# Optimization experiments

Hardware: AMD Instinct MI355X
Metric: run time of the kernel (lower is better)

## Reference

```python
import jax, jax.numpy as jnp
import numpy as np

N, D = 8192, 128

def setup_inputs() -> dict:
    key = jax.random.key(0)
    kq, kk, kv = jax.random.split(key, 3)
    return {
        "query": jax.random.normal(kq, (N, D), dtype=jnp.float32),
        "key": jax.random.normal(kk, (N, D), dtype=jnp.float32),
        "value": jax.random.normal(kv, (N, D), dtype=jnp.float32),
    }

def reference(query, key, value):
    # FlashAttentionV1 computes exact (non-causal, unmasked) softmax attention:
    # softmax(Q K^T / sqrt(d)) V, via tiled online softmax. The math is
    # identical to the dense formulation below.
    d = query.shape[-1]
    scores = jnp.einsum('qd,kd->qk', query, key) / jnp.sqrt(jnp.asarray(d, query.dtype))
    probs = jax.nn.softmax(scores, axis=-1)
    return jnp.einsum('qk,kd->qd', probs, value)
```

## Files before the change

### kernel.cpp

```cpp
#include <hip/hip_runtime.h>

#define NTOK 8192
#define DH   128
#define QBLK 128
#define KVB  64

typedef __attribute__((ext_vector_type(8)))  short bf16x8;
typedef __attribute__((ext_vector_type(16))) float f32x16;
typedef __attribute__((ext_vector_type(4)))  unsigned short u16x4;

typedef __attribute__((address_space(1))) const void gv_t;
typedef __attribute__((address_space(3))) void sv_t;

static __device__ __forceinline__ unsigned short f2bf(float x) {
  union { float f; unsigned int u; } a; a.f = x;
  unsigned int r = a.u + 0x7FFFu + ((a.u >> 16) & 1u);
  return (unsigned short)(r >> 16);
}

static __device__ __forceinline__ unsigned pk2(float lo, float hi) {
  unsigned r;
  asm("v_cvt_pk_bf16_f32 %0, %1, %2" : "=v"(r) : "v"(lo), "v"(hi));
  return r;
}

static __device__ __forceinline__ f32x16 zero16() {
  f32x16 v;
  #pragma unroll
  for (int i = 0; i < 16; ++i) v[i] = 0.f;
  return v;
}

__global__ __launch_bounds__(256)
void fa_prep(const float* __restrict__ Kg, const float* __restrict__ Vg,
             char* __restrict__ Kimg, char* __restrict__ Vimg)
{
  const int t = blockIdx.x;
  const int tid = threadIdx.x;

  {
    const int krow = tid >> 2;
    const int kcg  = (tid & 3) * 32;
    const float* src = Kg + ((size_t)t * KVB + krow) * DH + kcg;
    char* drow = Kimg + (size_t)t * 16384 + krow * 256;
    const int sw = (krow & 15) << 4;
    #pragma unroll
    for (int w = 0; w < 4; ++w) {
      float4 a = *reinterpret_cast<const float4*>(src + w * 8);
      float4 b = *reinterpret_cast<const float4*>(src + w * 8 + 4);
      union { bf16x8 v; unsigned short u[8]; } f;
      f.u[0] = f2bf(a.x); f.u[1] = f2bf(a.y); f.u[2] = f2bf(a.z); f.u[3] = f2bf(a.w);
      f.u[4] = f2bf(b.x); f.u[5] = f2bf(b.y); f.u[6] = f2bf(b.z); f.u[7] = f2bf(b.w);
      *reinterpret_cast<bf16x8*>(drow + ((kcg * 2 + w * 16) ^ sw)) = f.v;
    }
  }

  {
    #pragma unroll
    for (int it = 0; it < 2; ++it) {
      int task = tid + it * 256;
      int kvl  = (task & 15) * 4;
      int d0   = (task >> 4) * 4;
      const float* src = Vg + ((size_t)t * KVB + kvl) * DH + d0;
      float4 r0 = *reinterpret_cast<const float4*>(src);
      float4 r1 = *reinterpret_cast<const float4*>(src + DH);
      float4 r2 = *reinterpret_cast<const float4*>(src + 2 * DH);
      float4 r3 = *reinterpret_cast<const float4*>(src + 3 * DH);
      char* base = Vimg + (size_t)t * 16384;
      const int bb = kvl * 2;
      { int d = d0 + 0;
        u16x4 w4 = (u16x4){f2bf(r0.x), f2bf(r1.x), f2bf(r2.x), f2bf(r3.x)};
        *reinterpret_cast<u16x4*>(base + d * 128 + (bb ^ ((d & 15) << 3))) = w4; }
      { int d = d0 + 1;
        u16x4 w4 = (u16x4){f2bf(r0.y), f2bf(r1.y), f2bf(r2.y), f2bf(r3.y)};
        *reinterpret_cast<u16x4*>(base + d * 128 + (bb ^ ((d & 15) << 3))) = w4; }
      { int d = d0 + 2;
        u16x4 w4 = (u16x4){f2bf(r0.z), f2bf(r1.z), f2bf(r2.z), f2bf(r3.z)};
        *reinterpret_cast<u16x4*>(base + d * 128 + (bb ^ ((d & 15) << 3))) = w4; }
      { int d = d0 + 3;
        u16x4 w4 = (u16x4){f2bf(r0.w), f2bf(r1.w), f2bf(r2.w), f2bf(r3.w)};
        *reinterpret_cast<u16x4*>(base + d * 128 + (bb ^ ((d & 15) << 3))) = w4; }
    }
  }
}

static __device__ __forceinline__ void softmax_half(
    const f32x16& st, float& m_run, float& l_run, f32x16* oacc,
    bf16x8& pfa, bf16x8& pfb)
{
  float a0 = fmaxf(st[0],  st[1]),  a1 = fmaxf(st[2],  st[3]);
  float a2 = fmaxf(st[4],  st[5]),  a3 = fmaxf(st[6],  st[7]);
  float a4 = fmaxf(st[8],  st[9]),  a5 = fmaxf(st[10], st[11]);
  float a6 = fmaxf(st[12], st[13]), a7 = fmaxf(st[14], st[15]);
  float b0 = fmaxf(a0, a1), b1 = fmaxf(a2, a3);
  float b2 = fmaxf(a4, a5), b3 = fmaxf(a6, a7);
  float pmax = fmaxf(fmaxf(b0, b1), fmaxf(b2, b3));
  if (!__all(pmax <= m_run + 8.f)) {
    pmax = fmaxf(pmax, __shfl_xor(pmax, 32));
    const float m_new = fmaxf(m_run, pmax);
    const float corr  = (m_run > -1e30f) ? exp2f(m_run - m_new) : 0.f;
    l_run *= corr;
    #pragma unroll
    for (int i = 0; i < 4; ++i) oacc[i] = oacc[i] * corr;
    m_run = m_new;
  }
  float e[16];
  #pragma unroll
  for (int r = 0; r < 16; ++r) e[r] = exp2f(st[r] - m_run);
  float s0 = (e[0] + e[1])   + (e[2] + e[3]);
  float s1 = (e[4] + e[5])   + (e[6] + e[7]);
  float s2 = (e[8] + e[9])   + (e[10] + e[11]);
  float s3 = (e[12] + e[13]) + (e[14] + e[15]);
  l_run += (s0 + s1) + (s2 + s3);
  union { bf16x8 v; unsigned u[4]; } fa, fb;
  fa.u[0] = pk2(e[0],  e[1]);  fa.u[1] = pk2(e[2],  e[3]);
  fa.u[2] = pk2(e[4],  e[5]);  fa.u[3] = pk2(e[6],  e[7]);
  fb.u[0] = pk2(e[8],  e[9]);  fb.u[1] = pk2(e[10], e[11]);
  fb.u[2] = pk2(e[12], e[13]); fb.u[3] = pk2(e[14], e[15]);
  pfa = fa.v; pfb = fb.v;
}

__global__ __launch_bounds__(256, 2)
void fa_fwd(const float* __restrict__ Qg, const char* __restrict__ Kimg,
            const char* __restrict__ Vimg, float* __restrict__ Od,
            float* __restrict__ Mp, float* __restrict__ Lp,
            int ksplit, int chunk_len)
{
  __shared__ __align__(16) char smem[2][32768];
  const int tid  = threadIdx.x;
  const int lane = tid & 63;
  const int wv   = tid >> 6;
  const int l31  = lane & 31;
  const int hi   = lane >> 5;

  const int q0blk = blockIdx.x * QBLK;
  const int q     = q0blk + wv * 32 + l31;
  const int chunk = blockIdx.y;
  const float QSCALE = 0.1275313310087464f;

  const int tile0 = (chunk * chunk_len) >> 6;
  const int nst   = chunk_len >> 6;

  bf16x8 qf[8];
  {
    const float* qs = Qg + (size_t)q * DH + hi * 8;
    #pragma unroll
    for (int kc = 0; kc < 8; ++kc) {
      float4 a = *reinterpret_cast<const float4*>(qs + kc * 16);
      float4 b = *reinterpret_cast<const float4*>(qs + kc * 16 + 4);
      union { bf16x8 v; unsigned u[4]; } f;
      f.u[0] = pk2(a.x * QSCALE, a.y * QSCALE);
      f.u[1] = pk2(a.z * QSCALE, a.w * QSCALE);
      f.u[2] = pk2(b.x * QSCALE, b.y * QSCALE);
      f.u[3] = pk2(b.z * QSCALE, b.w * QSCALE);
      qf[kc] = f.v;
    }
  }

  const char* gbase = (wv < 2 ? Kimg : Vimg);
  const size_t goff = (size_t)(wv & 1) * 8192 + (size_t)lane * 16;
  const int    loff = (wv < 2 ? 0 : 16384) + (wv & 1) * 8192;

#define STAGE(B, T) do {                                                      \
    const char* _s = gbase + (size_t)(T) * 16384 + goff;                      \
    char* _d = &smem[B][loff];                                                \
    _Pragma("unroll")                                                         \
    for (int _i = 0; _i < 8; ++_i)                                            \
      __builtin_amdgcn_global_load_lds((gv_t*)(_s + _i * 1024),               \
                                       (sv_t*)(_d + _i * 1024), 16, 0, 0);    \
  } while (0)

  STAGE(0, tile0);
  if (nst > 1) STAGE(1, tile0 + 1);

  f32x16 oacc[4];
  #pragma unroll
  for (int i = 0; i < 4; ++i) oacc[i] = zero16();
  float m_run = -INFINITY, l_run = 0.f;

  int cur = 0;
  for (int t = 0; t < nst; ++t) {
    if (t + 1 < nst) asm volatile("s_waitcnt vmcnt(8)" ::: "memory");
    else             asm volatile("s_waitcnt vmcnt(0)" ::: "memory");
    __builtin_amdgcn_sched_barrier(0);
    __builtin_amdgcn_s_barrier();

    const char* smK = smem[cur];
    const char* smV = smem[cur] + 16384;
    const int swk = (l31 & 15) << 4;
    const int swv = (l31 & 15) << 3;

    f32x16 st0 = zero16(), st1 = zero16();
    __builtin_amdgcn_s_setprio(1);
    #pragma unroll
    for (int kc = 0; kc < 8; ++kc) {
      const int cb = (kc * 32 + hi * 16) ^ swk;
      bf16x8 a0 = *reinterpret_cast<const bf16x8*>(smK + l31 * 256 + cb);
      st0 = __builtin_amdgcn_mfma_f32_32x32x16_bf16(a0, qf[kc], st0, 0, 0, 0);
      bf16x8 a1 = *reinterpret_cast<const bf16x8*>(smK + (l31 + 32) * 256 + cb);
      st1 = __builtin_amdgcn_mfma_f32_32x32x16_bf16(a1, qf[kc], st1, 0, 0, 0);
    }
    __builtin_amdgcn_s_setprio(0);

    bf16x8 pf0a, pf0b;
    softmax_half(st0, m_run, l_run, oacc, pf0a, pf0b);
    __builtin_amdgcn_s_setprio(1);
    #pragma unroll
    for (int c = 0; c < 2; ++c) {
      const bf16x8 pb = c ? pf0b : pf0a;
      #pragma unroll
      for (int dt = 0; dt < 4; ++dt) {
        const char* vb = smV + (dt * 32 + l31) * 128;
        union { bf16x8 v; u16x4 h[2]; } a;
        a.h[0] = *reinterpret_cast<const u16x4*>(vb + ((c * 32 + 8 * hi) ^ swv));
        a.h[1] = *reinterpret_cast<const u16x4*>(vb + ((c * 32 + 16 + 8 * hi) ^ swv));
        oacc[dt] = __builtin_amdgcn_mfma_f32_32x32x16_bf16(a.v, pb, oacc[dt], 0, 0, 0);
      }
    }
    __builtin_amdgcn_s_setprio(0);

    bf16x8 pf1a, pf1b;
    softmax_half(st1, m_run, l_run, oacc, pf1a, pf1b);
    __builtin_amdgcn_s_setprio(1);
    #pragma unroll
    for (int c = 2; c < 4; ++c) {
      const bf16x8 pb = (c & 1) ? pf1b : pf1a;
      #pragma unroll
      for (int dt = 0; dt < 4; ++dt) {
        const char* vb = smV + (dt * 32 + l31) * 128;
        union { bf16x8 v; u16x4 h[2]; } a;
        a.h[0] = *reinterpret_cast<const u16x4*>(vb + ((c * 32 + 8 * hi) ^ swv));
        a.h[1] = *reinterpret_cast<const u16x4*>(vb + ((c * 32 + 16 + 8 * hi) ^ swv));
        oacc[dt] = __builtin_amdgcn_mfma_f32_32x32x16_bf16(a.v, pb, oacc[dt], 0, 0, 0);
      }
    }
    __builtin_amdgcn_s_setprio(0);

    __builtin_amdgcn_s_barrier();
    if (t + 2 < nst) STAGE(cur, tile0 + t + 2);
    cur ^= 1;
  }
#undef STAGE

  const float l_tot = l_run + __shfl_xor(l_run, 32);
  const float scale = (ksplit == 1) ? (1.f / l_tot) : 1.f;
  float* dstB = (ksplit == 1) ? Od : Od + (size_t)chunk * NTOK * DH;

  char* base = &smem[0][0] + wv * 16384;
  #pragma unroll
  for (int dt = 0; dt < 4; ++dt)
    #pragma unroll
    for (int rg = 0; rg < 4; ++rg)
      #pragma unroll
      for (int j = 0; j < 4; ++j) {
        const int d = dt * 32 + rg * 8 + hi * 4 + j;
        *reinterpret_cast<float*>(base + d * 128 + l31 * 4) =
            oacc[dt][rg * 4 + j] * scale;
      }
  asm volatile("s_waitcnt lgkmcnt(0)" ::: "memory");
  __builtin_amdgcn_sched_barrier(0);
  const int qloc4 = lane >> 2;
  const int s4    = lane & 3;
  #pragma unroll
  for (int qh = 0; qh < 2; ++qh) {
    const int qloc = qh * 16 + qloc4;
    float* dst = dstB + (size_t)(q0blk + wv * 32 + qloc) * DH;
    #pragma unroll
    for (int i = 0; i < 8; ++i) {
      const int dd = s4 * 4 + i * 16;
      float4 v;
      v.x = *reinterpret_cast<float*>(base + (dd + 0) * 128 + qloc * 4);
      v.y = *reinterpret_cast<float*>(base + (dd + 1) * 128 + qloc * 4);
      v.z = *reinterpret_cast<float*>(base + (dd + 2) * 128 + qloc * 4);
      v.w = *reinterpret_cast<float*>(base + (dd + 3) * 128 + qloc * 4);
      *reinterpret_cast<float4*>(dst + dd) = v;
    }
  }

  if (ksplit > 1 && lane < 32) {
    const int qg = q0blk + wv * 32 + lane;
    Mp[chunk * NTOK + qg] = m_run;
    Lp[chunk * NTOK + qg] = l_tot;
  }
}

__global__ __launch_bounds__(256)
void fa_combine(const float* __restrict__ Op, const float* __restrict__ Mp,
                const float* __restrict__ Lp, float* __restrict__ out, int ksplit)
{
  const int gid = blockIdx.x * 256 + threadIdx.x;
  const int q   = gid >> 5;
  const int dv  = (gid & 31) * 4;
  float mx = -INFINITY;
  for (int c = 0; c < ksplit; ++c) mx = fmaxf(mx, Mp[c * NTOK + q]);
  float den = 0.f;
  float ax = 0.f, ay = 0.f, az = 0.f, aw = 0.f;
  for (int c = 0; c < ksplit; ++c) {
    const float w = exp2f(Mp[c * NTOK + q] - mx);
    den += w * Lp[c * NTOK + q];
    float4 o = *reinterpret_cast<const float4*>(Op + (size_t)c * NTOK * DH + (size_t)q * DH + dv);
    ax += w * o.x; ay += w * o.y; az += w * o.z; aw += w * o.w;
  }
  const float r = 1.f / den;
  float4 res; res.x = ax * r; res.y = ay * r; res.z = az * r; res.w = aw * r;
  *reinterpret_cast<float4*>(out + (size_t)q * DH + dv) = res;
}

extern "C" void kernel_launch(void* const* d_in, const int* in_sizes, int n_in,
                              void* d_out, int out_size, void* d_ws, size_t ws_size,
                              hipStream_t stream)
{
  const float* Q = (const float*)d_in[0];
  const float* K = (const float*)d_in[1];
  const float* V = (const float*)d_in[2];
  float* out = (float*)d_out;

  auto need = [](size_t ks) {
    return ks * (size_t)NTOK * DH * 4 + 2 * ks * (size_t)NTOK * 4;
  };
  int KS = (ws_size >= need(8)) ? 8 : (ws_size >= need(4)) ? 4 : 2;

  char* Kimg = (char*)d_out;
  char* Vimg = Kimg + (size_t)NTOK * 256;

  float* Op = (float*)d_ws;
  float* Mp = Op + (size_t)KS * NTOK * DH;
  float* Lp = Mp + (size_t)KS * NTOK;

  fa_prep<<<NTOK / KVB, 256, 0, stream>>>(K, V, Kimg, Vimg);
  fa_fwd<<<dim3(NTOK / QBLK, KS), 256, 0, stream>>>(Q, Kimg, Vimg, Op, Mp, Lp,
                                                    KS, NTOK / KS);
  fa_combine<<<NTOK * DH / 4 / 256, 256, 0, stream>>>(Op, Mp, Lp, out, KS);
}
```

Baseline: 68.66 us.

## Shrink LDS to single-buffered V for 3 blocks/CU and raise KV split to 12

LDS per block drops from 64KB to 48KB by keeping K double-buffered and V single-buffered, with V loads issued one tile ahead and awaited by a mid-iteration barrier. Launch bounds go to 3 blocks per CU, and the KV split rises to 12 with uneven chunk sizes handled by a remainder-aware tile partition. Both softmax halves now run before a single PV MFMA phase, and the epilogue staging is serialized across wave pairs to fit the smaller LDS. The aim is more resident blocks and more grid parallelism. The cost is an extra barrier per tile, exposed V load latency, and more register pressure from the 3-block bound.

```diff
diff --git a/kernel.cpp b/kernel.cpp
--- a/kernel.cpp
+++ b/kernel.cpp
@@ -4,6 +4,7 @@
 #define DH   128
 #define QBLK 128
 #define KVB  64
+#define TILES (NTOK / KVB)
 
 typedef __attribute__((ext_vector_type(8)))  short bf16x8;
 typedef __attribute__((ext_vector_type(16))) float f32x16;
@@ -120,13 +121,12 @@
   pfa = fa.v; pfb = fb.v;
 }
 
-__global__ __launch_bounds__(256, 2)
+__global__ __launch_bounds__(256, 3)
 void fa_fwd(const float* __restrict__ Qg, const char* __restrict__ Kimg,
             const char* __restrict__ Vimg, float* __restrict__ Od,
-            float* __restrict__ Mp, float* __restrict__ Lp,
-            int ksplit, int chunk_len)
-{
-  __shared__ __align__(16) char smem[2][32768];
+            float* __restrict__ Mp, float* __restrict__ Lp, int ksplit)
+{
+  __shared__ __align__(16) char smem[49152];
   const int tid  = threadIdx.x;
   const int lane = tid & 63;
   const int wv   = tid >> 6;
@@ -138,8 +138,10 @@
   const int chunk = blockIdx.y;
   const float QSCALE = 0.1275313310087464f;
 
-  const int tile0 = (chunk * chunk_len) >> 6;
-  const int nst   = chunk_len >> 6;
+  const int bt    = TILES / ksplit;
+  const int rem   = TILES - bt * ksplit;
+  const int tile0 = chunk * bt + (chunk < rem ? chunk : rem);
+  const int nst   = bt + (chunk < rem ? 1 : 0);
 
   bf16x8 qf[8];
   {
@@ -159,19 +161,30 @@
 
   const char* gbase = (wv < 2 ? Kimg : Vimg);
   const size_t goff = (size_t)(wv & 1) * 8192 + (size_t)lane * 16;
-  const int    loff = (wv < 2 ? 0 : 16384) + (wv & 1) * 8192;
-
-#define STAGE(B, T) do {                                                      \
+  const int    lK   = (wv & 1) * 8192;
+  const int    lV   = 32768 + (wv & 1) * 8192;
+
+#define STAGE_K(B, T) do { if (wv < 2) {                                      \
     const char* _s = gbase + (size_t)(T) * 16384 + goff;                      \
-    char* _d = &smem[B][loff];                                                \
+    char* _d = &smem[(B) * 16384 + lK];                                       \
     _Pragma("unroll")                                                         \
     for (int _i = 0; _i < 8; ++_i)                                            \
       __builtin_amdgcn_global_load_lds((gv_t*)(_s + _i * 1024),               \
                                        (sv_t*)(_d + _i * 1024), 16, 0, 0);    \
-  } while (0)
-
-  STAGE(0, tile0);
-  if (nst > 1) STAGE(1, tile0 + 1);
+  } } while (0)
+
+#define STAGE_V(T) do { if (wv >= 2) {                                        \
+    const char* _s = gbase + (size_t)(T) * 16384 + goff;                      \
+    char* _d = &smem[lV];                                                     \
+    _Pragma("unroll")                                                         \
+    for (int _i = 0; _i < 8; ++_i)                                            \
+      __builtin_amdgcn_global_load_lds((gv_t*)(_s + _i * 1024),               \
+                                       (sv_t*)(_d + _i * 1024), 16, 0, 0);    \
+  } } while (0)
+
+  STAGE_K(0, tile0);
+  STAGE_K(1, tile0 + 1);
+  STAGE_V(tile0);
 
   f32x16 oacc[4];
   #pragma unroll
@@ -180,13 +193,15 @@
 
   int cur = 0;
   for (int t = 0; t < nst; ++t) {
-    if (t + 1 < nst) asm volatile("s_waitcnt vmcnt(8)" ::: "memory");
-    else             asm volatile("s_waitcnt vmcnt(0)" ::: "memory");
+    if (wv < 2) {
+      if (t + 1 < nst) asm volatile("s_waitcnt vmcnt(8)" ::: "memory");
+      else             asm volatile("s_waitcnt vmcnt(0)" ::: "memory");
+    }
     __builtin_amdgcn_sched_barrier(0);
     __builtin_amdgcn_s_barrier();
 
-    const char* smK = smem[cur];
-    const char* smV = smem[cur] + 16384;
+    const char* smK = &smem[cur * 16384];
+    const char* smV = &smem[32768];
     const int swk = (l31 & 15) << 4;
     const int swv = (l31 & 15) << 3;
 
@@ -202,12 +217,18 @@
     }
     __builtin_amdgcn_s_setprio(0);
 
-    bf16x8 pf0a, pf0b;
+    bf16x8 pf0a, pf0b, pf1a, pf1b;
     softmax_half(st0, m_run, l_run, oacc, pf0a, pf0b);
+    softmax_half(st1, m_run, l_run, oacc, pf1a, pf1b);
+
+    if (wv >= 2) asm volatile("s_waitcnt vmcnt(0)" ::: "memory");
+    __builtin_amdgcn_sched_barrier(0);
+    __builtin_amdgcn_s_barrier();
+
     __builtin_amdgcn_s_setprio(1);
     #pragma unroll
-    for (int c = 0; c < 2; ++c) {
-      const bf16x8 pb = c ? pf0b : pf0a;
+    for (int c = 0; c < 4; ++c) {
+      const bf16x8 pb = (c == 0) ? pf0a : (c == 1) ? pf0b : (c == 2) ? pf1a : pf1b;
       #pragma unroll
       for (int dt = 0; dt < 4; ++dt) {
         const char* vb = smV + (dt * 32 + l31) * 128;
@@ -219,61 +240,52 @@
     }
     __builtin_amdgcn_s_setprio(0);
 
-    bf16x8 pf1a, pf1b;
-    softmax_half(st1, m_run, l_run, oacc, pf1a, pf1b);
-    __builtin_amdgcn_s_setprio(1);
-    #pragma unroll
-    for (int c = 2; c < 4; ++c) {
-      const bf16x8 pb = (c & 1) ? pf1b : pf1a;
-      #pragma unroll
-      for (int dt = 0; dt < 4; ++dt) {
-        const char* vb = smV + (dt * 32 + l31) * 128;
-        union { bf16x8 v; u16x4 h[2]; } a;
-        a.h[0] = *reinterpret_cast<const u16x4*>(vb + ((c * 32 + 8 * hi) ^ swv));
-        a.h[1] = *reinterpret_cast<const u16x4*>(vb + ((c * 32 + 16 + 8 * hi) ^ swv));
-        oacc[dt] = __builtin_amdgcn_mfma_f32_32x32x16_bf16(a.v, pb, oacc[dt], 0, 0, 0);
-      }
-    }
-    __builtin_amdgcn_s_setprio(0);
-
     __builtin_amdgcn_s_barrier();
-    if (t + 2 < nst) STAGE(cur, tile0 + t + 2);
+    if (t + 2 < nst) STAGE_K(cur, tile0 + t + 2);
+    if (t + 1 < nst) STAGE_V(tile0 + t + 1);
     cur ^= 1;
   }
-#undef STAGE
+#undef STAGE_K
+#undef STAGE_V
 
   const float l_tot = l_run + __shfl_xor(l_run, 32);
   const float scale = (ksplit == 1) ? (1.f / l_tot) : 1.f;
   float* dstB = (ksplit == 1) ? Od : Od + (size_t)chunk * NTOK * DH;
 
-  char* base = &smem[0][0] + wv * 16384;
-  #pragma unroll
-  for (int dt = 0; dt < 4; ++dt)
-    #pragma unroll
-    for (int rg = 0; rg < 4; ++rg)
-      #pragma unroll
-      for (int j = 0; j < 4; ++j) {
-        const int d = dt * 32 + rg * 8 + hi * 4 + j;
-        *reinterpret_cast<float*>(base + d * 128 + l31 * 4) =
-            oacc[dt][rg * 4 + j] * scale;
-      }
-  asm volatile("s_waitcnt lgkmcnt(0)" ::: "memory");
-  __builtin_amdgcn_sched_barrier(0);
+  char* base = &smem[(wv & 1) * 16384];
   const int qloc4 = lane >> 2;
   const int s4    = lane & 3;
   #pragma unroll
-  for (int qh = 0; qh < 2; ++qh) {
-    const int qloc = qh * 16 + qloc4;
-    float* dst = dstB + (size_t)(q0blk + wv * 32 + qloc) * DH;
-    #pragma unroll
-    for (int i = 0; i < 8; ++i) {
-      const int dd = s4 * 4 + i * 16;
-      float4 v;
-      v.x = *reinterpret_cast<float*>(base + (dd + 0) * 128 + qloc * 4);
-      v.y = *reinterpret_cast<float*>(base + (dd + 1) * 128 + qloc * 4);
-      v.z = *reinterpret_cast<float*>(base + (dd + 2) * 128 + qloc * 4);
-      v.w = *reinterpret_cast<float*>(base + (dd + 3) * 128 + qloc * 4);
-      *reinterpret_cast<float4*>(dst + dd) = v;
+  for (int ph = 0; ph < 2; ++ph) {
+    __builtin_amdgcn_s_barrier();
+    if ((wv >> 1) == ph) {
+      #pragma unroll
+      for (int dt = 0; dt < 4; ++dt)
+        #pragma unroll
+        for (int rg = 0; rg < 4; ++rg)
+          #pragma unroll
+          for (int j = 0; j < 4; ++j) {
+            const int d = dt * 32 + rg * 8 + hi * 4 + j;
+            *reinterpret_cast<float*>(base + d * 128 + l31 * 4) =
+                oacc[dt][rg * 4 + j] * scale;
+          }
+      asm volatile("s_waitcnt lgkmcnt(0)" ::: "memory");
+      __builtin_amdgcn_sched_barrier(0);
+      #pragma unroll
+      for (int qh = 0; qh < 2; ++qh) {
+        const int qloc = qh * 16 + qloc4;
+        float* dst = dstB + (size_t)(q0blk + wv * 32 + qloc) * DH;
+        #pragma unroll
+        for (int i = 0; i < 8; ++i) {
+          const int dd = s4 * 4 + i * 16;
+          float4 v;
+          v.x = *reinterpret_cast<float*>(base + (dd + 0) * 128 + qloc * 4);
+          v.y = *reinterpret_cast<float*>(base + (dd + 1) * 128 + qloc * 4);
+          v.z = *reinterpret_cast<float*>(base + (dd + 2) * 128 + qloc * 4);
+          v.w = *reinterpret_cast<float*>(base + (dd + 3) * 128 + qloc * 4);
+          *reinterpret_cast<float4*>(dst + dd) = v;
+        }
+      }
     }
   }
 
@@ -318,7 +330,7 @@
   auto need = [](size_t ks) {
     return ks * (size_t)NTOK * DH * 4 + 2 * ks * (size_t)NTOK * 4;
   };
-  int KS = (ws_size >= need(8)) ? 8 : (ws_size >= need(4)) ? 4 : 2;
+  int KS = (ws_size >= need(12)) ? 12 : 8;
 
   char* Kimg = (char*)d_out;
   char* Vimg = Kimg + (size_t)NTOK * 256;
@@ -327,8 +339,7 @@
   float* Mp = Op + (size_t)KS * NTOK * DH;
   float* Lp = Mp + (size_t)KS * NTOK;
 
-  fa_prep<<<NTOK / KVB, 256, 0, stream>>>(K, V, Kimg, Vimg);
-  fa_fwd<<<dim3(NTOK / QBLK, KS), 256, 0, stream>>>(Q, Kimg, Vimg, Op, Mp, Lp,
-                                                    KS, NTOK / KS);
+  fa_prep<<<TILES, 256, 0, stream>>>(K, V, Kimg, Vimg);
+  fa_fwd<<<dim3(NTOK / QBLK, KS), 256, 0, stream>>>(Q, Kimg, Vimg, Op, Mp, Lp, KS);
   fa_combine<<<NTOK * DH / 4 / 256, 256, 0, stream>>>(Op, Mp, Lp, out, KS);
 }
```

Result: slower. 73.92 us (+7.7%).

## Process two 32-row query tiles per wave to reuse K/V LDS reads

Applied to the files above, without the earlier changes.

Each wave now handles 64 query rows (two 32-row MFMA tiles) instead of 32, doubling the query block to 256 per workgroup. Each K and V fragment read from LDS now feeds two MFMAs, which halves LDS traffic and global K/V staging per query. The cost is roughly double the accumulator and Q-fragment registers, so occupancy drops to one block per CU. The grid also has half as many query blocks, and the epilogue writes the two tiles one after the other through LDS.

```diff
diff --git a/kernel.cpp b/kernel.cpp
--- a/kernel.cpp
+++ b/kernel.cpp
@@ -2,7 +2,7 @@
 
 #define NTOK 8192
 #define DH   128
-#define QBLK 128
+#define QBLK 256
 #define KVB  64
 
 typedef __attribute__((ext_vector_type(8)))  short bf16x8;
@@ -120,7 +120,7 @@
   pfa = fa.v; pfb = fb.v;
 }
 
-__global__ __launch_bounds__(256, 2)
+__global__ __launch_bounds__(256, 1)
 void fa_fwd(const float* __restrict__ Qg, const char* __restrict__ Kimg,
             const char* __restrict__ Vimg, float* __restrict__ Od,
             float* __restrict__ Mp, float* __restrict__ Lp,
@@ -134,26 +134,35 @@
   const int hi   = lane >> 5;
 
   const int q0blk = blockIdx.x * QBLK;
-  const int q     = q0blk + wv * 32 + l31;
+  const int qA    = q0blk + wv * 64 + l31;
+  const int qB    = qA + 32;
   const int chunk = blockIdx.y;
   const float QSCALE = 0.1275313310087464f;
 
   const int tile0 = (chunk * chunk_len) >> 6;
   const int nst   = chunk_len >> 6;
 
-  bf16x8 qf[8];
+  bf16x8 qfA[8], qfB[8];
   {
-    const float* qs = Qg + (size_t)q * DH + hi * 8;
+    const float* qsA = Qg + (size_t)qA * DH + hi * 8;
+    const float* qsB = Qg + (size_t)qB * DH + hi * 8;
     #pragma unroll
     for (int kc = 0; kc < 8; ++kc) {
-      float4 a = *reinterpret_cast<const float4*>(qs + kc * 16);
-      float4 b = *reinterpret_cast<const float4*>(qs + kc * 16 + 4);
+      float4 a = *reinterpret_cast<const float4*>(qsA + kc * 16);
+      float4 b = *reinterpret_cast<const float4*>(qsA + kc * 16 + 4);
       union { bf16x8 v; unsigned u[4]; } f;
       f.u[0] = pk2(a.x * QSCALE, a.y * QSCALE);
       f.u[1] = pk2(a.z * QSCALE, a.w * QSCALE);
       f.u[2] = pk2(b.x * QSCALE, b.y * QSCALE);
       f.u[3] = pk2(b.z * QSCALE, b.w * QSCALE);
-      qf[kc] = f.v;
+      qfA[kc] = f.v;
+      float4 c = *reinterpret_cast<const float4*>(qsB + kc * 16);
+      float4 d = *reinterpret_cast<const float4*>(qsB + kc * 16 + 4);
+      f.u[0] = pk2(c.x * QSCALE, c.y * QSCALE);
+      f.u[1] = pk2(c.z * QSCALE, c.w * QSCALE);
+      f.u[2] = pk2(d.x * QSCALE, d.y * QSCALE);
+      f.u[3] = pk2(d.z * QSCALE, d.w * QSCALE);
+      qfB[kc] = f.v;
     }
   }
 
@@ -173,10 +182,11 @@
   STAGE(0, tile0);
   if (nst > 1) STAGE(1, tile0 + 1);
 
-  f32x16 oacc[4];
+  f32x16 oaccA[4], oaccB[4];
   #pragma unroll
-  for (int i = 0; i < 4; ++i) oacc[i] = zero16();
-  float m_run = -INFINITY, l_run = 0.f;
+  for (int i = 0; i < 4; ++i) { oaccA[i] = zero16(); oaccB[i] = zero16(); }
+  float mA = -INFINITY, lA = 0.f;
+  float mB = -INFINITY, lB = 0.f;
 
   int cur = 0;
   for (int t = 0; t < nst; ++t) {
@@ -190,48 +200,39 @@
     const int swk = (l31 & 15) << 4;
     const int swv = (l31 & 15) << 3;
 
-    f32x16 st0 = zero16(), st1 = zero16();
+    f32x16 sA0 = zero16(), sA1 = zero16(), sB0 = zero16(), sB1 = zero16();
     __builtin_amdgcn_s_setprio(1);
     #pragma unroll
     for (int kc = 0; kc < 8; ++kc) {
       const int cb = (kc * 32 + hi * 16) ^ swk;
       bf16x8 a0 = *reinterpret_cast<const bf16x8*>(smK + l31 * 256 + cb);
-      st0 = __builtin_amdgcn_mfma_f32_32x32x16_bf16(a0, qf[kc], st0, 0, 0, 0);
+      sA0 = __builtin_amdgcn_mfma_f32_32x32x16_bf16(a0, qfA[kc], sA0, 0, 0, 0);
+      sB0 = __builtin_amdgcn_mfma_f32_32x32x16_bf16(a0, qfB[kc], sB0, 0, 0, 0);
       bf16x8 a1 = *reinterpret_cast<const bf16x8*>(smK + (l31 + 32) * 256 + cb);
-      st1 = __builtin_amdgcn_mfma_f32_32x32x16_bf16(a1, qf[kc], st1, 0, 0, 0);
+      sA1 = __builtin_amdgcn_mfma_f32_32x32x16_bf16(a1, qfA[kc], sA1, 0, 0, 0);
+      sB1 = __builtin_amdgcn_mfma_f32_32x32x16_bf16(a1, qfB[kc], sB1, 0, 0, 0);
     }
     __builtin_amdgcn_s_setprio(0);
 
-    bf16x8 pf0a, pf0b;
-    softmax_half(st0, m_run, l_run, oacc, pf0a, pf0b);
+    bf16x8 pA0a, pA0b, pA1a, pA1b, pB0a, pB0b, pB1a, pB1b;
+    softmax_half(sA0, mA, lA, oaccA, pA0a, pA0b);
+    softmax_half(sA1, mA, lA, oaccA, pA1a, pA1b);
+    softmax_half(sB0, mB, lB, oaccB, pB0a, pB0b);
+    softmax_half(sB1, mB, lB, oaccB, pB1a, pB1b);
+
     __builtin_amdgcn_s_setprio(1);
     #pragma unroll
-    for (int c = 0; c < 2; ++c) {
-      const bf16x8 pb = c ? pf0b : pf0a;
+    for (int c = 0; c < 4; ++c) {
+      const bf16x8 pbA = (c == 0) ? pA0a : (c == 1) ? pA0b : (c == 2) ? pA1a : pA1b;
+      const bf16x8 pbB = (c == 0) ? pB0a : (c == 1) ? pB0b : (c == 2) ? pB1a : pB1b;
       #pragma unroll
       for (int dt = 0; dt < 4; ++dt) {
         const char* vb = smV + (dt * 32 + l31) * 128;
         union { bf16x8 v; u16x4 h[2]; } a;
         a.h[0] = *reinterpret_cast<const u16x4*>(vb + ((c * 32 + 8 * hi) ^ swv));
         a.h[1] = *reinterpret_cast<const u16x4*>(vb + ((c * 32 + 16 + 8 * hi) ^ swv));
-        oacc[dt] = __builtin_amdgcn_mfma_f32_32x32x16_bf16(a.v, pb, oacc[dt], 0, 0, 0);
-      }
-    }
-    __builtin_amdgcn_s_setprio(0);
-
-    bf16x8 pf1a, pf1b;
-    softmax_half(st1, m_run, l_run, oacc, pf1a, pf1b);
-    __builtin_amdgcn_s_setprio(1);
-    #pragma unroll
-    for (int c = 2; c < 4; ++c) {
-      const bf16x8 pb = (c & 1) ? pf1b : pf1a;
-      #pragma unroll
-      for (int dt = 0; dt < 4; ++dt) {
-        const char* vb = smV + (dt * 32 + l31) * 128;
-        union { bf16x8 v; u16x4 h[2]; } a;
-        a.h[0] = *reinterpret_cast<const u16x4*>(vb + ((c * 32 + 8 * hi) ^ swv));
-        a.h[1] = *reinterpret_cast<const u16x4*>(vb + ((c * 32 + 16 + 8 * hi) ^ swv));
-        oacc[dt] = __builtin_amdgcn_mfma_f32_32x32x16_bf16(a.v, pb, oacc[dt], 0, 0, 0);
+        oaccA[dt] = __builtin_amdgcn_mfma_f32_32x32x16_bf16(a.v, pbA, oaccA[dt], 0, 0, 0);
+        oaccB[dt] = __builtin_amdgcn_mfma_f32_32x32x16_bf16(a.v, pbB, oaccB[dt], 0, 0, 0);
       }
     }
     __builtin_amdgcn_s_setprio(0);
@@ -242,45 +243,58 @@
   }
 #undef STAGE
 
-  const float l_tot = l_run + __shfl_xor(l_run, 32);
-  const float scale = (ksplit == 1) ? (1.f / l_tot) : 1.f;
+  const float lAt = lA + __shfl_xor(lA, 32);
+  const float lBt = lB + __shfl_xor(lB, 32);
+  const float scA = (ksplit == 1) ? (1.f / lAt) : 1.f;
+  const float scB = (ksplit == 1) ? (1.f / lBt) : 1.f;
   float* dstB = (ksplit == 1) ? Od : Od + (size_t)chunk * NTOK * DH;
 
   char* base = &smem[0][0] + wv * 16384;
-  #pragma unroll
-  for (int dt = 0; dt < 4; ++dt)
-    #pragma unroll
-    for (int rg = 0; rg < 4; ++rg)
-      #pragma unroll
-      for (int j = 0; j < 4; ++j) {
-        const int d = dt * 32 + rg * 8 + hi * 4 + j;
-        *reinterpret_cast<float*>(base + d * 128 + l31 * 4) =
-            oacc[dt][rg * 4 + j] * scale;
-      }
-  asm volatile("s_waitcnt lgkmcnt(0)" ::: "memory");
-  __builtin_amdgcn_sched_barrier(0);
   const int qloc4 = lane >> 2;
   const int s4    = lane & 3;
-  #pragma unroll
-  for (int qh = 0; qh < 2; ++qh) {
-    const int qloc = qh * 16 + qloc4;
-    float* dst = dstB + (size_t)(q0blk + wv * 32 + qloc) * DH;
-    #pragma unroll
-    for (int i = 0; i < 8; ++i) {
-      const int dd = s4 * 4 + i * 16;
-      float4 v;
-      v.x = *reinterpret_cast<float*>(base + (dd + 0) * 128 + qloc * 4);
-      v.y = *reinterpret_cast<float*>(base + (dd + 1) * 128 + qloc * 4);
-      v.z = *reinterpret_cast<float*>(base + (dd + 2) * 128 + qloc * 4);
-      v.w = *reinterpret_cast<float*>(base + (dd + 3) * 128 + qloc * 4);
-      *reinterpret_cast<float4*>(dst + dd) = v;
-    }
-  }
+
+#define EPI(OACC, SC, QOFF) do {                                               \
+    _Pragma("unroll")                                                          \
+    for (int dt = 0; dt < 4; ++dt)                                             \
+      _Pragma("unroll")                                                        \
+      for (int rg = 0; rg < 4; ++rg)                                           \
+        _Pragma("unroll")                                                      \
+        for (int j = 0; j < 4; ++j) {                                          \
+          const int d = dt * 32 + rg * 8 + hi * 4 + j;                         \
+          *reinterpret_cast<float*>(base + d * 128 + l31 * 4) =                \
+              (OACC)[dt][rg * 4 + j] * (SC);                                   \
+        }                                                                      \
+    asm volatile("s_waitcnt lgkmcnt(0)" ::: "memory");                         \
+    __builtin_amdgcn_sched_barrier(0);                                         \
+    _Pragma("unroll")                                                          \
+    for (int qh = 0; qh < 2; ++qh) {                                           \
+      const int qloc = qh * 16 + qloc4;                                        \
+      float* dst = dstB + (size_t)(q0blk + wv * 64 + (QOFF) + qloc) * DH;      \
+      _Pragma("unroll")                                                        \
+      for (int i = 0; i < 8; ++i) {                                            \
+        const int dd = s4 * 4 + i * 16;                                        \
+        float4 v;                                                              \
+        v.x = *reinterpret_cast<float*>(base + (dd + 0) * 128 + qloc * 4);     \
+        v.y = *reinterpret_cast<float*>(base + (dd + 1) * 128 + qloc * 4);     \
+        v.z = *reinterpret_cast<float*>(base + (dd + 2) * 128 + qloc * 4);     \
+        v.w = *reinterpret_cast<float*>(base + (dd + 3) * 128 + qloc * 4);     \
+        *reinterpret_cast<float4*>(dst + dd) = v;                              \
+      }                                                                        \
+    }                                                                          \
+    asm volatile("s_waitcnt lgkmcnt(0)" ::: "memory");                         \
+    __builtin_amdgcn_sched_barrier(0);                                         \
+  } while (0)
+
+  EPI(oaccA, scA, 0);
+  EPI(oaccB, scB, 32);
+#undef EPI
 
   if (ksplit > 1 && lane < 32) {
-    const int qg = q0blk + wv * 32 + lane;
-    Mp[chunk * NTOK + qg] = m_run;
-    Lp[chunk * NTOK + qg] = l_tot;
+    const int qgA = q0blk + wv * 64 + lane;
+    Mp[chunk * NTOK + qgA] = mA;
+    Lp[chunk * NTOK + qgA] = lAt;
+    Mp[chunk * NTOK + qgA + 32] = mB;
+    Lp[chunk * NTOK + qgA + 32] = lBt;
   }
 }
 
```

Result: slower. 80.77 us (+17.6%).
